# Kernel tuning notes

Measured on AMD Instinct MI355X. Metric: run time of the kernel, lower is better.

Reference implementation:

```python
import jax, jax.numpy as jnp
import numpy as np

NUM_TERMS = 8
NUM_CHANNELS = 64
BATCH = 8
NODES = 2048


def setup_inputs() -> dict:
    key = jax.random.key(0)
    kA, kh = jax.random.split(key)
    A = jax.random.normal(kA, (BATCH, NODES, NODES), dtype=jnp.float32)
    # xavier_uniform over (num_terms+1, num_channels)
    fan_in, fan_out = NUM_TERMS + 1, NUM_CHANNELS
    limit = float(np.sqrt(6.0 / (fan_in + fan_out)))
    h = jax.random.uniform(kh, (NUM_TERMS + 1, NUM_CHANNELS), dtype=jnp.float32,
                           minval=-limit, maxval=limit)
    return {"A": A, "h": h}


def reference(A, h):
    # Y[b,n,c] = h[0,c] + sum_{i=1..T} h[i,c] * diag(A^i)[b,n]
    num_terms = h.shape[0] - 1
    diags = []  # each [B, N]: diagonal of A^i
    Ap = A
    for i in range(num_terms):
        if i > 0:
            Ap = jnp.matmul(Ap, A)  # A^(i+1), computed once per power
        diags.append(jnp.diagonal(Ap, axis1=-2, axis2=-1))
    D = jnp.stack(diags, axis=0)  # [T, B, N]
    # fuse per-channel weighted sum of diagonals into one einsum
    out = jnp.einsum("tbn,tc->bnc", D, h[1:])
    out = out + h[0][None, None, :]  # identity term: diag(I) == 1
    return out
```

## Files before the change

### kernel.cpp

```cpp
#include <hip/hip_runtime.h>
#include <hip/hip_bf16.h>

#define NN 2048
#define BB 8
#define NC 64
#define NTILE 32
#define NITER 16

typedef __bf16 bf16_8 __attribute__((ext_vector_type(8)));
typedef __bf16 bf16_4 __attribute__((ext_vector_type(4)));
typedef float f32x16 __attribute__((ext_vector_type(16)));

__device__ __forceinline__ void gll16(const void* g, void* l) {
  __builtin_amdgcn_global_load_lds((const __attribute__((address_space(1))) void*)g,
                                   (__attribute__((address_space(3))) void*)l,
                                   16, 0, 0);
}

__global__ __launch_bounds__(256)
void k_convert(const float* __restrict__ A, __bf16* __restrict__ Ab, __bf16* __restrict__ At) {
  __shared__ __bf16 tile[64][65];
  int b = blockIdx.z;
  const float* Asrc = A + (size_t)b * NN * NN;
  __bf16* Abd = Ab + (size_t)b * NN * NN;
  __bf16* Atd = At + (size_t)b * NN * NN;
  int r0 = blockIdx.y * 64, c0 = blockIdx.x * 64;
  int row = threadIdx.x >> 4;
  int col4 = (threadIdx.x & 15) * 4;
#pragma unroll
  for (int rr = 0; rr < 64; rr += 16) {
    float4 v = *(const float4*)&Asrc[(size_t)(r0 + row + rr) * NN + c0 + col4];
    bf16_4 hv;
    hv[0] = (__bf16)v.x; hv[1] = (__bf16)v.y; hv[2] = (__bf16)v.z; hv[3] = (__bf16)v.w;
    *(bf16_4*)&Abd[(size_t)(r0 + row + rr) * NN + c0 + col4] = hv;
    tile[row + rr][col4 + 0] = hv[0];
    tile[row + rr][col4 + 1] = hv[1];
    tile[row + rr][col4 + 2] = hv[2];
    tile[row + rr][col4 + 3] = hv[3];
  }
  __syncthreads();
  int row2 = threadIdx.x >> 3;
  int col8 = (threadIdx.x & 7) * 8;
#pragma unroll
  for (int rr = 0; rr < 64; rr += 32) {
    bf16_8 v;
#pragma unroll
    for (int j = 0; j < 8; ++j) v[j] = tile[col8 + j][row2 + rr];
    *(bf16_8*)&Atd[(size_t)(c0 + row2 + rr) * NN + r0 + col8] = v;
  }
}

__device__ __forceinline__
void gemm_body256(const __bf16* __restrict__ Pb, const __bf16* __restrict__ Qb,
                  __bf16* __restrict__ Cb, __bf16* __restrict__ Ctb,
                  __bf16* smem, int tmBlk, int tnBlk) {
  __bf16 (*As)[256][64] = (__bf16(*)[256][64])smem;
  __bf16 (*Bs)[256][64] = (__bf16(*)[256][64])(smem + 32768);
  const int tid = threadIdx.x;
  const int wave = tid >> 6, lane = tid & 63;
  const int wm = wave >> 2, wn = wave & 3;
  const int tm = tmBlk * 256, tn = tnBlk * 256;
  const int am = lane & 31, ah = lane >> 5;
  const int rx = (am >> 1) & 7;

  const int sr = lane >> 3;
  const int sc = (lane & 7) ^ (((wave & 1) * 4 + (lane >> 4)) & 7);
  const __bf16* srcA = Pb + (size_t)(tm + wave * 8 + sr) * NN + sc * 8;
  const __bf16* srcB = Qb + (size_t)(tn + wave * 8 + sr) * NN + sc * 8;

#define STAGE(Tc_, s_, bufT_)                                                  \
  do {                                                                         \
    if ((s_) == 0) {                                                 \
      const __bf16* s0 = srcA + (size_t)(Tc_) * 64;                            \
      gll16(s0,                   &As[bufT_][wave * 8][0]);                    \
      gll16(s0 + (size_t)64 * NN, &As[bufT_][64 + wave * 8][0]);               \
    } else if ((s_) == 1) {                                          \
      const __bf16* s0 = srcB + (size_t)128 * NN + (size_t)(Tc_) * 64;         \
      gll16(s0,                   &Bs[bufT_][128 + wave * 8][0]);              \
      gll16(s0 + (size_t)64 * NN, &Bs[bufT_][192 + wave * 8][0]);              \
    } else if ((s_) == 2) {                                          \
      const __bf16* s0 = srcA + (size_t)128 * NN + (size_t)(Tc_) * 64;         \
      gll16(s0,                   &As[bufT_][128 + wave * 8][0]);              \
      gll16(s0 + (size_t)64 * NN, &As[bufT_][192 + wave * 8][0]);              \
    } else {                                                         \
      const __bf16* s0 = srcB + (size_t)(Tc_) * 64;                            \
      gll16(s0,                   &Bs[bufT_][wave * 8][0]);                    \
      gll16(s0 + (size_t)64 * NN, &Bs[bufT_][64 + wave * 8][0]);               \
    }                                                                          \
  } while (0)

  STAGE(0, 0, 0); STAGE(0, 3, 0); STAGE(0, 1, 0); STAGE(0, 2, 0);
  STAGE(1, 0, 1); STAGE(1, 3, 1); STAGE(1, 1, 1);
  asm volatile("s_waitcnt vmcnt(6)" ::: "memory");
  __builtin_amdgcn_s_barrier();

  f32x16 acc[4][2] = {};
  bf16_8 af[2][4], bfr[2][4];

  for (int it = 0; it < NITER; ++it) {
#pragma unroll
    for (int h = 0; h < 2; ++h) {
      const int b = h;
#pragma unroll
      for (int ks = 0; ks < 4; ++ks) {
        const int ra = (0 * 2 + wm) * 32 + am;
        af[0][ks] = *(const bf16_8*)&As[b][ra][((2 * ks + ah) ^ rx) * 8];
      }
#pragma unroll
      for (int ks = 0; ks < 4; ++ks) {
        const int rb0 = wn * 32 + am;
        bfr[0][ks] = *(const bf16_8*)&Bs[b][rb0][((2 * ks + ah) ^ rx) * 8];
      }
#pragma unroll
      for (int ks = 0; ks < 4; ++ks) {
        const int ra = (1 * 2 + wm) * 32 + am;
        af[1][ks] = *(const bf16_8*)&As[b][ra][((2 * ks + ah) ^ rx) * 8];
      }
#pragma unroll
      for (int ks = 0; ks < 4; ++ks) {
        const int rb1 = (4 + wn) * 32 + am;
        bfr[1][ks] = *(const bf16_8*)&Bs[b][rb1][((2 * ks + ah) ^ rx) * 8];
      }
      {
        int T = 2 * it + h + 1; if (T > NTILE - 1) T = NTILE - 1;
        STAGE(T, 2, b ^ 1);
      }
      __builtin_amdgcn_s_setprio(1);
#pragma unroll
      for (int ks = 0; ks < 4; ++ks) {
#pragma unroll
        for (int i = 0; i < 2; ++i) {
          acc[i][0] = __builtin_amdgcn_mfma_f32_32x32x16_bf16(
              af[i][ks], bfr[0][ks], acc[i][0], 0, 0, 0);
          acc[i][1] = __builtin_amdgcn_mfma_f32_32x32x16_bf16(
              af[i][ks], bfr[1][ks], acc[i][1], 0, 0, 0);
        }
      }
      __builtin_amdgcn_s_setprio(0);
      __builtin_amdgcn_sched_barrier(0);
      __builtin_amdgcn_s_barrier();
#pragma unroll
      for (int i = 0; i < 2; ++i) {
        const int ra = (4 + 2 * i + wm) * 32 + am;
#pragma unroll
        for (int ks = 0; ks < 4; ++ks)
          af[i][ks] = *(const bf16_8*)&As[b][ra][((2 * ks + ah) ^ rx) * 8];
      }
      {
        int T = 2 * it + h + 2; if (T > NTILE - 1) T = NTILE - 1;
        STAGE(T, 0, b); STAGE(T, 3, b); STAGE(T, 1, b);
      }
      __builtin_amdgcn_s_setprio(1);
#pragma unroll
      for (int ks = 0; ks < 4; ++ks) {
#pragma unroll
        for (int i = 0; i < 2; ++i) {
          acc[2 + i][1] = __builtin_amdgcn_mfma_f32_32x32x16_bf16(
              af[i][ks], bfr[1][ks], acc[2 + i][1], 0, 0, 0);
          acc[2 + i][0] = __builtin_amdgcn_mfma_f32_32x32x16_bf16(
              af[i][ks], bfr[0][ks], acc[2 + i][0], 0, 0, 0);
        }
      }
      __builtin_amdgcn_s_setprio(0);
      asm volatile("s_waitcnt vmcnt(6)" ::: "memory");
      __builtin_amdgcn_sched_barrier(0);
      __builtin_amdgcn_s_barrier();
    }
  }
  asm volatile("s_waitcnt vmcnt(0) lgkmcnt(0)" ::: "memory");

  const int cc = am;
  const int rq = ah * 4;
#pragma unroll
  for (int im = 0; im < 4; ++im)
#pragma unroll
    for (int in = 0; in < 2; ++in)
#pragma unroll
      for (int reg = 0; reg < 16; ++reg) {
        int row = (reg & 3) + 8 * (reg >> 2) + rq;
        Cb[(size_t)(tm + (2 * im + wm) * 32 + row) * NN +
           (tn + (4 * in + wn) * 32 + cc)] = (__bf16)acc[im][in][reg];
      }

  if (Ctb != nullptr) {
    __syncthreads();
    __bf16 (*Tt)[264] = (__bf16(*)[264])smem;
#pragma unroll
    for (int ch = 0; ch < 4; ++ch) {
      if ((wn >> 1) == (ch & 1)) {
        const int inw = ch >> 1;
#pragma unroll
        for (int im = 0; im < 4; ++im)
#pragma unroll
          for (int g = 0; g < 4; ++g) {
            bf16_4 v;
#pragma unroll
            for (int r = 0; r < 4; ++r) v[r] = (__bf16)acc[im][inw][g * 4 + r];
            *(bf16_4*)&Tt[(wn & 1) * 32 + cc][(2 * im + wm) * 32 + 8 * g + rq] = v;
          }
      }
      __syncthreads();
#pragma unroll
      for (int rr = 0; rr < 4; ++rr) {
        int trow = rr * 16 + (tid >> 5);
        int tcol = (tid & 31) * 8;
        bf16_8 v = *(const bf16_8*)&Tt[trow][tcol];
        *(bf16_8*)&Ctb[(size_t)(tn + ch * 64 + trow) * NN + tm + tcol] = v;
      }
      __syncthreads();
    }
  }
#undef STAGE
}


__global__ __launch_bounds__(512, 2)
void k_gemm1(const __bf16* __restrict__ Ab, const __bf16* __restrict__ At,
             __bf16* __restrict__ A2, __bf16* __restrict__ A2t) {
  __shared__ __align__(16) __bf16 smem[65536];
  int lid = ((int)blockIdx.z * gridDim.y + blockIdx.y) * gridDim.x + blockIdx.x;
  int swz = (lid & 7) * 64 + (lid >> 3);
  int bz = swz >> 6, ty = (swz >> 3) & 7, tx = swz & 7;
  size_t mb = (size_t)bz * NN * NN;
  gemm_body256(Ab + mb, At + mb, A2 + mb, A2t + mb, smem, ty, tx);
}

__global__ __launch_bounds__(512, 2)
void k_gemm23(const __bf16* __restrict__ At, const __bf16* __restrict__ A2,
              const __bf16* __restrict__ A2t,
              __bf16* __restrict__ A3t, __bf16* __restrict__ A4,
              __bf16* __restrict__ A4t) {
  __shared__ __align__(16) __bf16 smem[65536];
  int lid = ((int)blockIdx.z * gridDim.y + blockIdx.y) * gridDim.x + blockIdx.x;
  int swz = (lid & 7) * 128 + (lid >> 3);
  int bz = swz >> 6, ty = (swz >> 3) & 7, tx = swz & 7;
  int job = bz >> 3;
  size_t mb = (size_t)(bz & 7) * NN * NN;
  if (job == 0)
    gemm_body256(At + mb, A2 + mb, A3t + mb, nullptr, smem, ty, tx);
  else
    gemm_body256(A2 + mb, A2t + mb, A4 + mb, A4t + mb, smem, ty, tx);
}

__global__ __launch_bounds__(256)
void k_reduce(const float* __restrict__ A, const float* __restrict__ h,
              const __bf16* __restrict__ A2, const __bf16* __restrict__ A3t,
              const __bf16* __restrict__ A4, const __bf16* __restrict__ A4t,
              float* __restrict__ out) {
  int b = blockIdx.y;
  int wave = threadIdx.x >> 6, lane = threadIdx.x & 63;
  int n = blockIdx.x * 4 + wave;
  size_t mb = (size_t)b * NN * NN;
  size_t rb = mb + (size_t)n * NN;
  float d5 = 0, d6 = 0, d7 = 0, d8 = 0;
  for (int c = 0; c < NN; c += 512) {
    int k = c + lane * 8;
    bf16_8 va2  = *(const bf16_8*)(A2 + rb + k);
    bf16_8 va3t = *(const bf16_8*)(A3t + rb + k);
    bf16_8 va4  = *(const bf16_8*)(A4 + rb + k);
    bf16_8 va4t = *(const bf16_8*)(A4t + rb + k);
#pragma unroll
    for (int j = 0; j < 8; ++j) {
      float f2 = (float)va2[j], f4 = (float)va4[j];
      float f3t = (float)va3t[j], f4t = (float)va4t[j];
      d5 += f2 * f3t;
      d6 += f2 * f4t;
      d7 += f4 * f3t;
      d8 += f4 * f4t;
    }
  }
#pragma unroll
  for (int off = 32; off > 0; off >>= 1) {
    d5 += __shfl_xor(d5, off);
    d6 += __shfl_xor(d6, off);
    d7 += __shfl_xor(d7, off);
    d8 += __shfl_xor(d8, off);
  }
  float d1 = A[mb + (size_t)n * NN + n];
  float d2 = (float)A2[rb + n];
  float d3 = (float)A3t[rb + n];
  float d4 = (float)A4[rb + n];
  float r = h[lane] + h[64 + lane] * d1 + h[128 + lane] * d2 + h[192 + lane] * d3 +
            h[256 + lane] * d4 + h[320 + lane] * d5 + h[384 + lane] * d6 +
            h[448 + lane] * d7 + h[512 + lane] * d8;
  out[((size_t)b * NN + n) * NC + lane] = r;
}

extern "C" void kernel_launch(void* const* d_in, const int* in_sizes, int n_in,
                              void* d_out, int out_size, void* d_ws, size_t ws_size,
                              hipStream_t stream) {
  const float* A = (const float*)d_in[0];
  const float* h = (const float*)d_in[1];
  float* out = (float*)d_out;

  size_t elems = (size_t)BB * NN * NN;
  __bf16* Ab  = (__bf16*)d_ws;
  __bf16* At  = Ab + elems;
  __bf16* A2  = At + elems;
  __bf16* A2t = A2 + elems;
  __bf16* A3t = A2t + elems;
  __bf16* A4  = A3t + elems;
  __bf16* A4t = Ab;

  k_convert<<<dim3(32, 32, BB), dim3(256), 0, stream>>>(A, Ab, At);
  k_gemm1<<<dim3(8, 8, BB), dim3(512), 0, stream>>>(Ab, At, A2, A2t);
  k_gemm23<<<dim3(8, 8, 2 * BB), dim3(512), 0, stream>>>(At, A2, A2t, A3t, A4, A4t);
  k_reduce<<<dim3(NN / 4, BB), dim3(256), 0, stream>>>(A, h, A2, A3t, A4, A4t, out);
}
```

Baseline: 645.5 us.

## Compute A^4 and A^6 transposes and recover odd diagonals in reduce

Changes the power chain from A2, A3t, A4 to A2, A4t = A2·A2 and A6t = A2·A4, using a new transpose-only GEMM kernel that skips the row-major store. The reduce kernel rebuilds diag(A^3), diag(A^5), diag(A^7) and diag(A^8) as row-column dot products over A, At, A2, A4t and A6t. This cuts one full matrix write from the GEMM stage and drops the A4t aliasing over Ab. In exchange, the second-stage GEMMs become two dependent launches instead of one larger batched launch, and the reduce kernel reads five matrices instead of four.

```diff
diff --git a/kernel.cpp b/kernel.cpp
--- a/kernel.cpp
+++ b/kernel.cpp
@@ -171,16 +171,18 @@
 
   const int cc = am;
   const int rq = ah * 4;
-#pragma unroll
-  for (int im = 0; im < 4; ++im)
-#pragma unroll
-    for (int in = 0; in < 2; ++in)
-#pragma unroll
-      for (int reg = 0; reg < 16; ++reg) {
-        int row = (reg & 3) + 8 * (reg >> 2) + rq;
-        Cb[(size_t)(tm + (2 * im + wm) * 32 + row) * NN +
-           (tn + (4 * in + wn) * 32 + cc)] = (__bf16)acc[im][in][reg];
-      }
+  if (Cb != nullptr) {
+#pragma unroll
+    for (int im = 0; im < 4; ++im)
+#pragma unroll
+      for (int in = 0; in < 2; ++in)
+#pragma unroll
+        for (int reg = 0; reg < 16; ++reg) {
+          int row = (reg & 3) + 8 * (reg >> 2) + rq;
+          Cb[(size_t)(tm + (2 * im + wm) * 32 + row) * NN +
+             (tn + (4 * in + wn) * 32 + cc)] = (__bf16)acc[im][in][reg];
+        }
+  }
 
   if (Ctb != nullptr) {
     __syncthreads();
@@ -226,60 +228,55 @@
 }
 
 __global__ __launch_bounds__(512, 2)
-void k_gemm23(const __bf16* __restrict__ At, const __bf16* __restrict__ A2,
-              const __bf16* __restrict__ A2t,
-              __bf16* __restrict__ A3t, __bf16* __restrict__ A4,
-              __bf16* __restrict__ A4t) {
+void k_gemmT(const __bf16* __restrict__ P, const __bf16* __restrict__ Q,
+             __bf16* __restrict__ Ct) {
   __shared__ __align__(16) __bf16 smem[65536];
   int lid = ((int)blockIdx.z * gridDim.y + blockIdx.y) * gridDim.x + blockIdx.x;
-  int swz = (lid & 7) * 128 + (lid >> 3);
+  int swz = (lid & 7) * 64 + (lid >> 3);
   int bz = swz >> 6, ty = (swz >> 3) & 7, tx = swz & 7;
-  int job = bz >> 3;
-  size_t mb = (size_t)(bz & 7) * NN * NN;
-  if (job == 0)
-    gemm_body256(At + mb, A2 + mb, A3t + mb, nullptr, smem, ty, tx);
-  else
-    gemm_body256(A2 + mb, A2t + mb, A4 + mb, A4t + mb, smem, ty, tx);
+  size_t mb = (size_t)bz * NN * NN;
+  gemm_body256(P + mb, Q + mb, nullptr, Ct + mb, smem, ty, tx);
 }
 
 __global__ __launch_bounds__(256)
 void k_reduce(const float* __restrict__ A, const float* __restrict__ h,
-              const __bf16* __restrict__ A2, const __bf16* __restrict__ A3t,
-              const __bf16* __restrict__ A4, const __bf16* __restrict__ A4t,
-              float* __restrict__ out) {
+              const __bf16* __restrict__ Ab, const __bf16* __restrict__ At,
+              const __bf16* __restrict__ A2, const __bf16* __restrict__ A4t,
+              const __bf16* __restrict__ A6t, float* __restrict__ out) {
   int b = blockIdx.y;
   int wave = threadIdx.x >> 6, lane = threadIdx.x & 63;
   int n = blockIdx.x * 4 + wave;
   size_t mb = (size_t)b * NN * NN;
   size_t rb = mb + (size_t)n * NN;
-  float d5 = 0, d6 = 0, d7 = 0, d8 = 0;
+  float d3 = 0, d5 = 0, d7 = 0, d8 = 0;
   for (int c = 0; c < NN; c += 512) {
     int k = c + lane * 8;
-    bf16_8 va2  = *(const bf16_8*)(A2 + rb + k);
-    bf16_8 va3t = *(const bf16_8*)(A3t + rb + k);
-    bf16_8 va4  = *(const bf16_8*)(A4 + rb + k);
-    bf16_8 va4t = *(const bf16_8*)(A4t + rb + k);
+    bf16_8 vab = *(const bf16_8*)(Ab + rb + k);
+    bf16_8 vat = *(const bf16_8*)(At + rb + k);
+    bf16_8 va2 = *(const bf16_8*)(A2 + rb + k);
+    bf16_8 v4t = *(const bf16_8*)(A4t + rb + k);
+    bf16_8 v6t = *(const bf16_8*)(A6t + rb + k);
 #pragma unroll
     for (int j = 0; j < 8; ++j) {
-      float f2 = (float)va2[j], f4 = (float)va4[j];
-      float f3t = (float)va3t[j], f4t = (float)va4t[j];
-      d5 += f2 * f3t;
-      d6 += f2 * f4t;
-      d7 += f4 * f3t;
-      d8 += f4 * f4t;
+      float fab = (float)vab[j], fat = (float)vat[j], f2 = (float)va2[j];
+      float f4t = (float)v4t[j], f6t = (float)v6t[j];
+      d3 += f2 * fat;
+      d5 += fab * f4t;
+      d7 += fab * f6t;
+      d8 += f2 * f6t;
     }
   }
 #pragma unroll
   for (int off = 32; off > 0; off >>= 1) {
+    d3 += __shfl_xor(d3, off);
     d5 += __shfl_xor(d5, off);
-    d6 += __shfl_xor(d6, off);
     d7 += __shfl_xor(d7, off);
     d8 += __shfl_xor(d8, off);
   }
   float d1 = A[mb + (size_t)n * NN + n];
   float d2 = (float)A2[rb + n];
-  float d3 = (float)A3t[rb + n];
-  float d4 = (float)A4[rb + n];
+  float d4 = (float)A4t[rb + n];
+  float d6 = (float)A6t[rb + n];
   float r = h[lane] + h[64 + lane] * d1 + h[128 + lane] * d2 + h[192 + lane] * d3 +
             h[256 + lane] * d4 + h[320 + lane] * d5 + h[384 + lane] * d6 +
             h[448 + lane] * d7 + h[512 + lane] * d8;
@@ -298,12 +295,13 @@
   __bf16* At  = Ab + elems;
   __bf16* A2  = At + elems;
   __bf16* A2t = A2 + elems;
-  __bf16* A3t = A2t + elems;
-  __bf16* A4  = A3t + elems;
-  __bf16* A4t = Ab;
-
+  __bf16* A4t = A2t + elems;
+  __bf16* A6t = A4t + elems;
+
+  dim3 g512(8, 8, BB), b512(512);
   k_convert<<<dim3(32, 32, BB), dim3(256), 0, stream>>>(A, Ab, At);
-  k_gemm1<<<dim3(8, 8, BB), dim3(512), 0, stream>>>(Ab, At, A2, A2t);
-  k_gemm23<<<dim3(8, 8, 2 * BB), dim3(512), 0, stream>>>(At, A2, A2t, A3t, A4, A4t);
-  k_reduce<<<dim3(NN / 4, BB), dim3(256), 0, stream>>>(A, h, A2, A3t, A4, A4t, out);
-}
+  k_gemm1<<<g512, b512, 0, stream>>>(Ab, At, A2, A2t);
+  k_gemmT<<<g512, b512, 0, stream>>>(A2, A2t, A4t);
+  k_gemmT<<<g512, b512, 0, stream>>>(A2, A4t, A6t);
+  k_reduce<<<dim3(NN / 4, BB), dim3(256), 0, stream>>>(A, h, Ab, At, A2, A4t, A6t, out);
+}
```

Measured after the change: 658.9 us. 2.1% more time.
